# Kernel tuning notes

Measured on AMD Instinct MI355X. Metric: run time of the kernel, lower is better.

The kernel has to match this reference:

```python
import jax, jax.numpy as jnp
import numpy as np

NUM_Q = 500000
NUM_E = 250000
DIM = 256
HEADS = 4
NEG_SLOPE = 0.01
EPS = 1e-16


def setup_inputs() -> dict:
    key = jax.random.key(0)
    k1, k2, k3, k4, k5 = jax.random.split(key, 5)
    x_q = jax.random.normal(k1, (NUM_Q, DIM), dtype=jnp.float32)
    x_edge = jax.random.normal(k2, (NUM_E, DIM), dtype=jnp.float32)
    edge_ids = jax.random.randint(k3, (NUM_Q,), 0, NUM_E, dtype=jnp.int64)
    # learned params: w_q (input_dim, output_dim), attention weight (H, 2*dim/H)
    w_q = jax.random.normal(k4, (DIM, DIM), dtype=jnp.float32) / np.sqrt(DIM)
    weight = jax.random.normal(k5, (HEADS, 2 * DIM // HEADS), dtype=jnp.float32) / np.sqrt(2 * DIM // HEADS)
    return {"x_q": x_q, "x_edge": x_edge, "w_q": w_q, "weight": weight, "edge_ids": edge_ids}


def reference(x_q, x_edge, w_q, weight, edge_ids):
    nq = x_q.shape[0]
    ne = x_edge.shape[0]
    h = weight.shape[0]
    # project qualifier pairs: (nq, dim) -> (nq, H, d_head)
    xq = (x_q @ w_q).reshape(nq, h, -1)
    # gather edge reps per qualifier pair: (nq, H, d_head)
    xe = x_edge[edge_ids].reshape(nq, h, -1)
    # per-head attention logits: eh
    alpha = jnp.einsum('ehd,hd->eh', jnp.concatenate([xe, xq], axis=-1), weight)
    alpha = jax.nn.leaky_relu(alpha, NEG_SLOPE)
    # segment softmax grouped by edge_ids (numerically stable)
    seg_max = jax.ops.segment_max(alpha, edge_ids, num_segments=ne)
    seg_max = jnp.where(jnp.isfinite(seg_max), seg_max, 0.0)  # empty segments
    ex = jnp.exp(alpha - seg_max[edge_ids])
    seg_sum = jax.ops.segment_sum(ex, edge_ids, num_segments=ne)
    alpha = ex / (seg_sum[edge_ids] + EPS)
    # weight qualifier reps and scatter-add to edges
    xq = (alpha[..., None] * xq).reshape(nq, -1)
    return jax.ops.segment_sum(xq, edge_ids, num_segments=ne)
```

## Files before the change

### kernel.cpp

```cpp
#include <hip/hip_runtime.h>
#include <hip/hip_bf16.h>

#define DIM 256
#define HEADS 4
#define NEG_SLOPE 0.01f

typedef unsigned short u16;
typedef __attribute__((ext_vector_type(8))) short short8;
typedef __attribute__((ext_vector_type(4))) float f32x4;

__device__ __forceinline__ u16 f2bf(float f) {
    unsigned u = __float_as_uint(f);
    unsigned r = (u + 0x7fffu + ((u >> 16) & 1u)) >> 16;
    return (u16)r;
}
__device__ __forceinline__ unsigned cvt2(float a, float b) {
    __hip_bfloat162 h = __float22bfloat162_rn(make_float2(a, b));
    unsigned u;
    __builtin_memcpy(&u, &h, 4);
    return u;
}

__global__ __launch_bounds__(256) void prepb_kernel(const float* __restrict__ B,
                                                    u16* __restrict__ BThi) {
    int k = blockIdx.x;
    int n = threadIdx.x;
    BThi[n * 256 + k] = f2bf(B[k * 256 + n]);
}

__global__ __launch_bounds__(256) void prepwg_kernel(const float* __restrict__ wq,
                                                     const float* __restrict__ weight,
                                                     float* __restrict__ wg) {
    int k = threadIdx.x;
#pragma unroll
    for (int h = 0; h < 4; ++h) {
        float s = 0.f;
        for (int d = 0; d < 64; ++d)
            s = fmaf(wq[k * 256 + h * 64 + d], weight[h * 128 + 64 + d], s);
        wg[k * 4 + h] = s;
    }
}

__global__ __launch_bounds__(256) void beta_kernel(const float* __restrict__ xe,
                                                   const float* __restrict__ weight,
                                                   float* __restrict__ beta, int NE) {
    int wid = blockIdx.x * 4 + (threadIdx.x >> 6);
    if (wid >= NE) return;
    int lane = threadIdx.x & 63;
    int h = lane >> 4;
    float4 v = *reinterpret_cast<const float4*>(xe + (size_t)wid * DIM + lane * 4);
    float4 w = *reinterpret_cast<const float4*>(weight + h * 128 + (lane & 15) * 4);
    float p = v.x * w.x + v.y * w.y + v.z * w.z + v.w * w.w;
    p += __shfl_xor(p, 1);
    p += __shfl_xor(p, 2);
    p += __shfl_xor(p, 4);
    p += __shfl_xor(p, 8);
    if ((lane & 15) == 0) beta[(size_t)wid * 4 + h] = p;
}

__global__ __launch_bounds__(256) void gamma_kernel(const float* __restrict__ xq,
                                                    const float* __restrict__ wg,
                                                    const float* __restrict__ beta,
                                                    const int* __restrict__ eids,
                                                    float* __restrict__ exv,
                                                    float* __restrict__ segsum,
                                                    unsigned* __restrict__ counts, int NQ) {
    int e = blockIdx.x * 4 + (threadIdx.x >> 6);
    if (e >= NQ) return;
    int lane = threadIdx.x & 63;
    float4 x = *reinterpret_cast<const float4*>(xq + (size_t)e * DIM + lane * 4);
    float4 p = make_float4(0.f, 0.f, 0.f, 0.f);
    const float xs[4] = {x.x, x.y, x.z, x.w};
#pragma unroll
    for (int i = 0; i < 4; ++i) {
        float4 w = *reinterpret_cast<const float4*>(wg + (lane * 4 + i) * 4);
        p.x = fmaf(xs[i], w.x, p.x);
        p.y = fmaf(xs[i], w.y, p.y);
        p.z = fmaf(xs[i], w.z, p.z);
        p.w = fmaf(xs[i], w.w, p.w);
    }
#pragma unroll
    for (int d = 1; d < 64; d <<= 1) {
        p.x += __shfl_xor(p.x, d);
        p.y += __shfl_xor(p.y, d);
        p.z += __shfl_xor(p.z, d);
        p.w += __shfl_xor(p.w, d);
    }
    if (lane == 0) {
        int j = eids[e];
        float4 b = *reinterpret_cast<const float4*>(beta + (size_t)j * 4);
        float l[4] = {b.x + p.x, b.y + p.y, b.z + p.z, b.w + p.w};
        float ex[4];
#pragma unroll
        for (int h = 0; h < 4; ++h) {
            l[h] = l[h] > 0.f ? l[h] : NEG_SLOPE * l[h];
            ex[h] = __expf(l[h]);
        }
        *reinterpret_cast<float4*>(exv + (size_t)e * 4) = make_float4(ex[0], ex[1], ex[2], ex[3]);
#pragma unroll
        for (int h = 0; h < 4; ++h) atomicAdd(&segsum[(size_t)j * 4 + h], ex[h]);
        atomicAdd(&counts[j], 1u);
    }
}

__global__ __launch_bounds__(256) void scan1_kernel(const unsigned* __restrict__ counts,
                                                    unsigned* __restrict__ offs,
                                                    unsigned* __restrict__ blocksums, int NE) {
    __shared__ unsigned s[256];
    int t = threadIdx.x;
    int base = blockIdx.x * 1024 + t * 4;
    unsigned v[4], sum = 0;
#pragma unroll
    for (int i = 0; i < 4; ++i) {
        v[i] = (base + i < NE) ? counts[base + i] : 0u;
        sum += v[i];
    }
    s[t] = sum;
    __syncthreads();
    for (int off = 1; off < 256; off <<= 1) {
        unsigned y = (t >= off) ? s[t - off] : 0u;
        __syncthreads();
        s[t] += y;
        __syncthreads();
    }
    unsigned excl = s[t] - sum;
#pragma unroll
    for (int i = 0; i < 4; ++i) {
        if (base + i < NE) offs[base + i] = excl;
        excl += v[i];
    }
    if (t == 255) blocksums[blockIdx.x] = s[255];
}

__global__ __launch_bounds__(256) void scan2_kernel(unsigned* __restrict__ blocksums, int NB) {
    __shared__ unsigned s[256];
    int t = threadIdx.x;
    unsigned v = (t < NB) ? blocksums[t] : 0u;
    s[t] = v;
    __syncthreads();
    for (int off = 1; off < 256; off <<= 1) {
        unsigned y = (t >= off) ? s[t - off] : 0u;
        __syncthreads();
        s[t] += y;
        __syncthreads();
    }
    if (t < NB) blocksums[t] = s[t] - v;
}

__global__ __launch_bounds__(256) void scan3_kernel(unsigned* __restrict__ offs,
                                                    const unsigned* __restrict__ blocksums,
                                                    unsigned* __restrict__ cursor, int NE) {
    int t = threadIdx.x;
    int base = blockIdx.x * 1024 + t * 4;
    unsigned add = blocksums[blockIdx.x];
#pragma unroll
    for (int i = 0; i < 4; ++i) {
        if (base + i < NE) {
            unsigned o = offs[base + i] + add;
            offs[base + i] = o;
            cursor[base + i] = o;
        }
    }
}

__global__ __launch_bounds__(256) void fill_kernel(const int* __restrict__ eids,
                                                   unsigned* __restrict__ cursor,
                                                   int* __restrict__ qlist, int NQ) {
    int e = blockIdx.x * blockDim.x + threadIdx.x;
    if (e >= NQ) return;
    int j = eids[e];
    unsigned pos = atomicAdd(&cursor[j], 1u);
    qlist[pos] = e;
}

__global__ __launch_bounds__(512, 4) void aggmm_kernel(const float* __restrict__ xq,
                                                       const u16* __restrict__ BThi,
                                                       const float* __restrict__ exv,
                                                       const float* __restrict__ segsum,
                                                       const unsigned* __restrict__ offs,
                                                       const unsigned* __restrict__ counts,
                                                       const int* __restrict__ qlist,
                                                       float* __restrict__ out, int NE) {
    __shared__ u16 agg_s[64 * 256];

    const int t = threadIdx.x;
    const int w = t >> 6;
    const int lane = t & 63;

    for (int e2 = 0; e2 < 2; ++e2) {
        const int e_loc = w * 2 + e2;
        const long j = (long)blockIdx.x * 16 + e_loc;
        f32x4 a0 = (f32x4){0.f, 0.f, 0.f, 0.f};
        f32x4 a1 = a0, a2 = a0, a3 = a0;
        if (j < NE) {
            const unsigned beg = offs[j];
            const unsigned n = counts[j];
            float4 ss = *reinterpret_cast<const float4*>(segsum + (size_t)j * 4);
            const float inv0 = 1.f / (ss.x + 1e-16f);
            const float inv1 = 1.f / (ss.y + 1e-16f);
            const float inv2 = 1.f / (ss.z + 1e-16f);
            const float inv3 = 1.f / (ss.w + 1e-16f);
            const float* xcol = xq + lane * 4;
#pragma unroll 2
            for (unsigned i = 0; i < n; ++i) {
                int q = qlist[beg + i];
                float4 e4 = *reinterpret_cast<const float4*>(exv + (size_t)q * 4);
                float4 xv = *reinterpret_cast<const float4*>(xcol + (size_t)q * DIM);
                f32x4 xvv = {xv.x, xv.y, xv.z, xv.w};
                a0 += (e4.x * inv0) * xvv;
                a1 += (e4.y * inv1) * xvv;
                a2 += (e4.z * inv2) * xvv;
                a3 += (e4.w * inv3) * xvv;
            }
        }
        const int halfsel = (lane & 1) * 4;
        f32x4 accs[4] = {a0, a1, a2, a3};
#pragma unroll
        for (int h = 0; h < 4; ++h) {
            int row = e_loc * 4 + h;
            int chunk = (lane >> 1) ^ (row & 7);
            uint2 wv = make_uint2(cvt2(accs[h][0], accs[h][1]), cvt2(accs[h][2], accs[h][3]));
            *reinterpret_cast<uint2*>(&agg_s[row * 256 + chunk * 8 + halfsel]) = wv;
        }
    }
    __syncthreads();

    const int h = w >> 1;
    const int gp = w & 1;
    const int lr = lane & 15;
    const int kg = lane >> 4;
    const int rowA = lr * 4 + h;
    const u16* bptr0 = BThi + (h * 64 + gp * 32 + lr) * 256 + kg * 8;
    const u16* bptr1 = bptr0 + 16 * 256;

    f32x4 cc0 = (f32x4){0.f, 0.f, 0.f, 0.f};
    f32x4 cc1 = cc0;
#pragma unroll
    for (int s = 0; s < 8; ++s) {
        int phys = (s * 4 + kg) ^ (rowA & 7);
        short8 ah = *reinterpret_cast<const short8*>(&agg_s[rowA * 256 + phys * 8]);
        short8 b0 = *reinterpret_cast<const short8*>(bptr0 + s * 32);
        short8 b1 = *reinterpret_cast<const short8*>(bptr1 + s * 32);
        cc0 = __builtin_amdgcn_mfma_f32_16x16x32_bf16(ah, b0, cc0, 0, 0, 0);
        cc1 = __builtin_amdgcn_mfma_f32_16x16x32_bf16(ah, b1, cc1, 0, 0, 0);
    }
#pragma unroll
    for (int r = 0; r < 4; ++r) {
        long jj = (long)blockIdx.x * 16 + kg * 4 + r;
        if (jj < NE) {
            float* orow = out + jj * DIM + h * 64 + gp * 32 + lr;
            orow[0]  = cc0[r];
            orow[16] = cc1[r];
        }
    }
}

extern "C" void kernel_launch(void* const* d_in, const int* in_sizes, int n_in,
                              void* d_out, int out_size, void* d_ws, size_t ws_size,
                              hipStream_t stream) {
    (void)n_in; (void)out_size; (void)ws_size;
    const float* x_q    = (const float*)d_in[0];
    const float* x_edge = (const float*)d_in[1];
    const float* w_q    = (const float*)d_in[2];
    const float* weight = (const float*)d_in[3];
    const int*   eids   = (const int*)d_in[4];
    const int NQ = in_sizes[0] / DIM;
    const int NE = in_sizes[1] / DIM;
    float* out = (float*)d_out;

    float*    exv       = (float*)d_ws;
    float*    beta      = exv + (size_t)NQ * 4;
    float*    segsum    = beta + (size_t)NE * 4;
    unsigned* counts    = (unsigned*)(segsum + (size_t)NE * 4);
    unsigned* offs      = counts + NE;
    unsigned* cursor    = offs + NE;
    int*      qlist     = (int*)(cursor + NE);
    unsigned* blocksums = (unsigned*)(qlist + NQ);
    u16*      BThi      = (u16*)(blocksums + 256);
    float*    wg        = (float*)(BThi + 256 * 256);

    const int NB = (NE + 1023) / 1024;

    hipMemsetAsync(segsum, 0, (size_t)NE * 4 * sizeof(float), stream);
    hipMemsetAsync(counts, 0, (size_t)NE * sizeof(unsigned), stream);

    prepb_kernel<<<256, 256, 0, stream>>>(w_q, BThi);
    prepwg_kernel<<<1, 256, 0, stream>>>(w_q, weight, wg);
    beta_kernel<<<(NE + 3) / 4, 256, 0, stream>>>(x_edge, weight, beta, NE);
    gamma_kernel<<<(NQ + 3) / 4, 256, 0, stream>>>(x_q, wg, beta, eids, exv, segsum, counts, NQ);
    scan1_kernel<<<NB, 256, 0, stream>>>(counts, offs, blocksums, NE);
    scan2_kernel<<<1, 256, 0, stream>>>(blocksums, NB);
    scan3_kernel<<<NB, 256, 0, stream>>>(offs, blocksums, cursor, NE);
    fill_kernel<<<(NQ + 255) / 256, 256, 0, stream>>>(eids, cursor, qlist, NQ);
    aggmm_kernel<<<(NE + 15) / 16, 512, 0, stream>>>(x_q, BThi, exv, segsum, offs, counts,
                                                     qlist, out, NE);
}
```

Baseline: 681.8 us.

## Fuse attention logit and softmax computation into the per-edge aggregation kernel

Removes the separate gamma pass, which read all of x_q, wrote per-qualifier exp values and atomically accumulated segment sums. Logits, exponentials and segment sums are now computed inside the aggregation kernel from the x_q rows it already gathers. Up to six rows per edge are kept in registers so they are read once. This drops a full read of x_q, the exv buffer, the segsum memset and the atomics. In exchange it adds more registers, per-row shuffle reductions, and a second x_q read for edges with more than six qualifiers.

```diff
diff --git a/kernel.cpp b/kernel.cpp
--- a/kernel.cpp
+++ b/kernel.cpp
@@ -4,6 +4,7 @@
 #define DIM 256
 #define HEADS 4
 #define NEG_SLOPE 0.01f
+#define ROWS_REG 6
 
 typedef unsigned short u16;
 typedef __attribute__((ext_vector_type(8))) short short8;
@@ -58,49 +59,11 @@
     if ((lane & 15) == 0) beta[(size_t)wid * 4 + h] = p;
 }
 
-__global__ __launch_bounds__(256) void gamma_kernel(const float* __restrict__ xq,
-                                                    const float* __restrict__ wg,
-                                                    const float* __restrict__ beta,
-                                                    const int* __restrict__ eids,
-                                                    float* __restrict__ exv,
-                                                    float* __restrict__ segsum,
+__global__ __launch_bounds__(256) void count_kernel(const int* __restrict__ eids,
                                                     unsigned* __restrict__ counts, int NQ) {
-    int e = blockIdx.x * 4 + (threadIdx.x >> 6);
+    int e = blockIdx.x * blockDim.x + threadIdx.x;
     if (e >= NQ) return;
-    int lane = threadIdx.x & 63;
-    float4 x = *reinterpret_cast<const float4*>(xq + (size_t)e * DIM + lane * 4);
-    float4 p = make_float4(0.f, 0.f, 0.f, 0.f);
-    const float xs[4] = {x.x, x.y, x.z, x.w};
-#pragma unroll
-    for (int i = 0; i < 4; ++i) {
-        float4 w = *reinterpret_cast<const float4*>(wg + (lane * 4 + i) * 4);
-        p.x = fmaf(xs[i], w.x, p.x);
-        p.y = fmaf(xs[i], w.y, p.y);
-        p.z = fmaf(xs[i], w.z, p.z);
-        p.w = fmaf(xs[i], w.w, p.w);
-    }
-#pragma unroll
-    for (int d = 1; d < 64; d <<= 1) {
-        p.x += __shfl_xor(p.x, d);
-        p.y += __shfl_xor(p.y, d);
-        p.z += __shfl_xor(p.z, d);
-        p.w += __shfl_xor(p.w, d);
-    }
-    if (lane == 0) {
-        int j = eids[e];
-        float4 b = *reinterpret_cast<const float4*>(beta + (size_t)j * 4);
-        float l[4] = {b.x + p.x, b.y + p.y, b.z + p.z, b.w + p.w};
-        float ex[4];
-#pragma unroll
-        for (int h = 0; h < 4; ++h) {
-            l[h] = l[h] > 0.f ? l[h] : NEG_SLOPE * l[h];
-            ex[h] = __expf(l[h]);
-        }
-        *reinterpret_cast<float4*>(exv + (size_t)e * 4) = make_float4(ex[0], ex[1], ex[2], ex[3]);
-#pragma unroll
-        for (int h = 0; h < 4; ++h) atomicAdd(&segsum[(size_t)j * 4 + h], ex[h]);
-        atomicAdd(&counts[j], 1u);
-    }
+    atomicAdd(&counts[eids[e]], 1u);
 }
 
 __global__ __launch_bounds__(256) void scan1_kernel(const unsigned* __restrict__ counts,
@@ -173,10 +136,10 @@
     qlist[pos] = e;
 }
 
-__global__ __launch_bounds__(512, 4) void aggmm_kernel(const float* __restrict__ xq,
+__global__ __launch_bounds__(512, 4) void fused_kernel(const float* __restrict__ xq,
                                                        const u16* __restrict__ BThi,
-                                                       const float* __restrict__ exv,
-                                                       const float* __restrict__ segsum,
+                                                       const float* __restrict__ wg,
+                                                       const float* __restrict__ beta,
                                                        const unsigned* __restrict__ offs,
                                                        const unsigned* __restrict__ counts,
                                                        const int* __restrict__ qlist,
@@ -187,6 +150,7 @@
     const int w = t >> 6;
     const int lane = t & 63;
 
+#pragma unroll 1
     for (int e2 = 0; e2 < 2; ++e2) {
         const int e_loc = w * 2 + e2;
         const long j = (long)blockIdx.x * 16 + e_loc;
@@ -195,22 +159,80 @@
         if (j < NE) {
             const unsigned beg = offs[j];
             const unsigned n = counts[j];
-            float4 ss = *reinterpret_cast<const float4*>(segsum + (size_t)j * 4);
-            const float inv0 = 1.f / (ss.x + 1e-16f);
-            const float inv1 = 1.f / (ss.y + 1e-16f);
-            const float inv2 = 1.f / (ss.z + 1e-16f);
-            const float inv3 = 1.f / (ss.w + 1e-16f);
+            const unsigned nn = n < ROWS_REG ? n : ROWS_REG;
+            const float4 b4 = *reinterpret_cast<const float4*>(beta + (size_t)j * 4);
             const float* xcol = xq + lane * 4;
-#pragma unroll 2
-            for (unsigned i = 0; i < n; ++i) {
+
+            auto gamma_ex = [&](float4 xv) -> float4 {
+                float4 p = make_float4(0.f, 0.f, 0.f, 0.f);
+                const float xs[4] = {xv.x, xv.y, xv.z, xv.w};
+#pragma unroll
+                for (int c = 0; c < 4; ++c) {
+                    float4 wr = *reinterpret_cast<const float4*>(wg + (lane * 4 + c) * 4);
+                    p.x = fmaf(xs[c], wr.x, p.x);
+                    p.y = fmaf(xs[c], wr.y, p.y);
+                    p.z = fmaf(xs[c], wr.z, p.z);
+                    p.w = fmaf(xs[c], wr.w, p.w);
+                }
+#pragma unroll
+                for (int d = 1; d < 64; d <<= 1) {
+                    p.x += __shfl_xor(p.x, d);
+                    p.y += __shfl_xor(p.y, d);
+                    p.z += __shfl_xor(p.z, d);
+                    p.w += __shfl_xor(p.w, d);
+                }
+                float l0 = b4.x + p.x, l1 = b4.y + p.y, l2 = b4.z + p.z, l3 = b4.w + p.w;
+                l0 = l0 > 0.f ? l0 : NEG_SLOPE * l0;
+                l1 = l1 > 0.f ? l1 : NEG_SLOPE * l1;
+                l2 = l2 > 0.f ? l2 : NEG_SLOPE * l2;
+                l3 = l3 > 0.f ? l3 : NEG_SLOPE * l3;
+                return make_float4(__expf(l0), __expf(l1), __expf(l2), __expf(l3));
+            };
+
+            float4 xr[ROWS_REG];
+            float4 exr[ROWS_REG];
+#pragma unroll
+            for (int i = 0; i < ROWS_REG; ++i)
+                if ((unsigned)i < nn) {
+                    int q = qlist[beg + i];
+                    xr[i] = *reinterpret_cast<const float4*>(xcol + (size_t)q * DIM);
+                }
+            float4 ssum = make_float4(0.f, 0.f, 0.f, 0.f);
+#pragma unroll
+            for (int i = 0; i < ROWS_REG; ++i)
+                if ((unsigned)i < nn) {
+                    float4 e = gamma_ex(xr[i]);
+                    exr[i] = e;
+                    ssum.x += e.x; ssum.y += e.y; ssum.z += e.z; ssum.w += e.w;
+                }
+            for (unsigned i = ROWS_REG; i < n; ++i) {
                 int q = qlist[beg + i];
-                float4 e4 = *reinterpret_cast<const float4*>(exv + (size_t)q * 4);
                 float4 xv = *reinterpret_cast<const float4*>(xcol + (size_t)q * DIM);
+                float4 e = gamma_ex(xv);
+                ssum.x += e.x; ssum.y += e.y; ssum.z += e.z; ssum.w += e.w;
+            }
+            const float inv0 = 1.f / (ssum.x + 1e-16f);
+            const float inv1 = 1.f / (ssum.y + 1e-16f);
+            const float inv2 = 1.f / (ssum.z + 1e-16f);
+            const float inv3 = 1.f / (ssum.w + 1e-16f);
+#pragma unroll
+            for (int i = 0; i < ROWS_REG; ++i)
+                if ((unsigned)i < nn) {
+                    f32x4 xvv = {xr[i].x, xr[i].y, xr[i].z, xr[i].w};
+                    a0 += (exr[i].x * inv0) * xvv;
+                    a1 += (exr[i].y * inv1) * xvv;
+                    a2 += (exr[i].z * inv2) * xvv;
+                    a3 += (exr[i].w * inv3) * xvv;
+                }
+            for (unsigned i = ROWS_REG; i < n; ++i) {
+                int q = qlist[beg + i];
+                float4 xv = *reinterpret_cast<const float4*>(xcol + (size_t)q * DIM);
+                float4 e = gamma_ex(xv);
                 f32x4 xvv = {xv.x, xv.y, xv.z, xv.w};
-                a0 += (e4.x * inv0) * xvv;
-                a1 += (e4.y * inv1) * xvv;
-                a2 += (e4.z * inv2) * xvv;
-                a3 += (e4.w * inv3) * xvv;
+                a0 += (e.x * inv0) * xvv;
+                a1 += (e.y * inv1) * xvv;
+                a2 += (e.z * inv2) * xvv;
+                a3 += (e.w * inv3) * xvv;
             }
         }
         const int halfsel = (lane & 1) * 4;
@@ -268,10 +290,8 @@
     const int NE = in_sizes[1] / DIM;
     float* out = (float*)d_out;
 
-    float*    exv       = (float*)d_ws;
-    float*    beta      = exv + (size_t)NQ * 4;
-    float*    segsum    = beta + (size_t)NE * 4;
-    unsigned* counts    = (unsigned*)(segsum + (size_t)NE * 4);
+    float*    beta      = (float*)d_ws;
+    unsigned* counts    = (unsigned*)(beta + (size_t)NE * 4);
     unsigned* offs      = counts + NE;
     unsigned* cursor    = offs + NE;
     int*      qlist     = (int*)(cursor + NE);
@@ -281,17 +301,16 @@
 
     const int NB = (NE + 1023) / 1024;
 
-    hipMemsetAsync(segsum, 0, (size_t)NE * 4 * sizeof(float), stream);
     hipMemsetAsync(counts, 0, (size_t)NE * sizeof(unsigned), stream);
 
     prepb_kernel<<<256, 256, 0, stream>>>(w_q, BThi);
     prepwg_kernel<<<1, 256, 0, stream>>>(w_q, weight, wg);
     beta_kernel<<<(NE + 3) / 4, 256, 0, stream>>>(x_edge, weight, beta, NE);
-    gamma_kernel<<<(NQ + 3) / 4, 256, 0, stream>>>(x_q, wg, beta, eids, exv, segsum, counts, NQ);
+    count_kernel<<<(NQ + 255) / 256, 256, 0, stream>>>(eids, counts, NQ);
     scan1_kernel<<<NB, 256, 0, stream>>>(counts, offs, blocksums, NE);
     scan2_kernel<<<1, 256, 0, stream>>>(blocksums, NB);
     scan3_kernel<<<NB, 256, 0, stream>>>(offs, blocksums, cursor, NE);
     fill_kernel<<<(NQ + 255) / 256, 256, 0, stream>>>(eids, cursor, qlist, NQ);
-    aggmm_kernel<<<(NE + 15) / 16, 512, 0, stream>>>(x_q, BThi, exv, segsum, offs, counts,
+    fused_kernel<<<(NE + 15) / 16, 512, 0, stream>>>(x_q, BThi, wg, beta, offs, counts,
                                                      qlist, out, NE);
 }
```

Result: slower. 714.9 us (+4.9%).
